# Kernel optimization log

Measured on AMD Instinct MI355X. Metric: run time of the kernel, lower is better.

The kernel has to match this reference:

```python
import jax, jax.numpy as jnp
import numpy as np

B = 4096


def setup_inputs() -> dict:
    key = jax.random.key(0)
    u = jax.random.uniform(key, (B, 5), dtype=jnp.float32)
    centers = u[:, :2] * 64.0          # box centers in [0, 64)
    wh = u[:, 2:4] * 8.0 + 1.0         # widths/heights in [1, 9)
    ang = u[:, 4:5] * 3.14159265       # rotation angle in [0, pi)
    boxes = jnp.concatenate([centers, wh, ang], axis=-1)  # (B,5)
    return {"boxes": boxes}


def _rect_to_corners(boxes):
    # boxes: (B,5) = (x, y, w, h, theta) -> corners (B,4,2)
    unit = jnp.array([[-1.0, -1.0], [1.0, -1.0], [1.0, 1.0], [-1.0, 1.0]],
                     dtype=boxes.dtype)
    ctr, wh, ang = boxes[:, :2], boxes[:, 2:4], boxes[:, 4]
    base = unit[None, :, :] * (wh * 0.5)[:, None, :]        # (B,4,2)
    c, s = jnp.cos(ang), jnp.sin(ang)
    rot = jnp.stack([jnp.stack([c, -s], -1),
                     jnp.stack([s, c], -1)], axis=1)         # (B,2,2)
    return jnp.einsum('bkd,bde->bke', base, rot) + ctr[:, None, :]


def _giou1d(min1, max1, min2, max2):
    # exact (non-fast) 1-D GIoU per axis
    inter = jnp.clip(jnp.minimum(max1, max2) - jnp.maximum(min1, min2), 0.0)
    union = (max1 - min1) + (max2 - min2) - inter
    hull = jnp.maximum(max1, max2) - jnp.minimum(min1, min2)
    return inter / union - (hull - union) / hull


def reference(boxes):
    corners = _rect_to_corners(boxes)                        # (B,4,2)
    nb = corners.shape[0]
    # two edge axes per box: c1-c0 and c3-c0
    axes = jnp.stack([corners[:, 1] - corners[:, 0],
                      corners[:, 3] - corners[:, 0]], axis=1)  # (B,2,2)
    # self projections: box b's corners onto its own axes
    sp = jnp.einsum('bkd,bad->bak', corners, axes)           # (B,2,4)
    smin, smax = sp.min(-1), sp.max(-1)                      # (B,2)
    # cross projections: corners of box i onto axes of box j
    cp = jnp.einsum('ikd,jad->ijak', corners, axes)          # (B,B,2,4)
    cmin, cmax = cp.min(-1), cp.max(-1)                      # (B,B,2)
    # projections of box j's corners onto box i's axes = transpose of cross
    cminT, cmaxT = jnp.swapaxes(cmin, 0, 1), jnp.swapaxes(cmax, 0, 1)
    # axes of box i: (box i self) vs (box j projected on i's axes)
    gA = _giou1d(smin[:, None, :], smax[:, None, :], cminT, cmaxT)  # (B,B,2)
    # axes of box j: (box i projected on j's axes) vs (box j self)
    gB = _giou1d(cmin, cmax, smin[None, :, :], smax[None, :, :])    # (B,B,2)
    g = jnp.concatenate([gA, gB], axis=-1).min(-1)           # min over 4 axes
    pairwise = jnp.clip(g, 0.0)
    idx = jnp.arange(nb)
    pairwise = pairwise.at[idx, idx].set(0.0)                # zero diagonal
    return pairwise  # reduction='none' -> (B,B)
```

## Files before the change

kernel.cpp:

```cpp
#include <hip/hip_runtime.h>
#include <math.h>

#define NBOX 4096
#define TILE 32
#define NT (NBOX / TILE)
#define NBLK (NT * (NT + 1) / 2)
#define SS 12
#define JBASE (TILE * SS)


struct Box {
    float cx, cy, a0x, a0y, a1x, a1y, sc0, sc1, l0, l1;
};

__device__ __forceinline__ float rcp_fast(float x) {
    return __builtin_amdgcn_rcpf(x);
}

__device__ __forceinline__ float giou_axis1(float H1, float H2, float D) {
    float S = H1 + H2;
    float u = fmaf(0.5f, S, -fabsf(D));
    float r = fminf(fminf(H1, H2), u);
    return r * rcp_fast(S - r);
}

__device__ __forceinline__ float mgiou_pair(const Box& I, const Box& J) {
    float d00 = fmaf(I.a0x, J.a0x, I.a0y * J.a0y);
    float d01 = fmaf(I.a0x, J.a1x, I.a0y * J.a1y);
    float d10 = fmaf(I.a1x, J.a0x, I.a1y * J.a0y);
    float d11 = fmaf(I.a1x, J.a1x, I.a1y * J.a1y);
    float DI0 = fmaf(I.a0x, J.cx, fmaf(I.a0y, J.cy, -I.sc0));
    float DI1 = fmaf(I.a1x, J.cx, fmaf(I.a1y, J.cy, -I.sc1));
    float DJ0 = fmaf(J.a0x, I.cx, fmaf(J.a0y, I.cy, -J.sc0));
    float DJ1 = fmaf(J.a1x, I.cx, fmaf(J.a1y, I.cy, -J.sc1));
    float HI0 = fabsf(d00) + fabsf(d01);
    float HI1 = fabsf(d10) + fabsf(d11);
    float HJ0 = fabsf(d00) + fabsf(d10);
    float HJ1 = fabsf(d01) + fabsf(d11);
    float g0 = giou_axis1(I.l0, HI0, DI0);
    float g1 = giou_axis1(I.l1, HI1, DI1);
    float g2 = giou_axis1(J.l0, HJ0, DJ0);
    float g3 = giou_axis1(J.l1, HJ1, DJ1);
    float g = fminf(fminf(g0, g1), fminf(g2, g3));
    return fmaxf(g, 0.0f);
}

__device__ __forceinline__ int j_offset(int j) {
    return JBASE + j * SS + (j >> 3) * 4;
}

__device__ __forceinline__ Box load_box(const float* p) {
    Box b;
    float4 x = *(const float4*)(p);
    float4 y = *(const float4*)(p + 4);
    float2 z = *(const float2*)(p + 8);
    b.cx = x.x;  b.cy = x.y;  b.a0x = x.z; b.a0y = x.w;
    b.a1x = y.x; b.a1y = y.y; b.sc0 = y.z; b.sc1 = y.w;
    b.l0 = z.x;  b.l1 = z.y;
    return b;
}

__global__ __launch_bounds__(256)
void pairwise_kernel(const float* __restrict__ boxes, float* __restrict__ out) {
    int k = blockIdx.x;
    int bi = (int)((float)(2 * NT + 1 - sqrtf((float)((2 * NT + 1) * (2 * NT + 1) - 8 * k))) * 0.5f);
    if (bi > 0 && k < bi * NT - bi * (bi - 1) / 2) bi--;
    if (k >= (bi + 1) * NT - (bi + 1) * bi / 2) bi++;
    int bj = bi + (k - (bi * NT - bi * (bi - 1) / 2));

    __shared__ float sm[JBASE + TILE * SS + 16];
    __shared__ float tileT[TILE][TILE + 1];

    int tid = threadIdx.x;
    if (tid < 2 * TILE) {
        int loc = (tid < TILE) ? tid : (tid - TILE);
        int box = (tid < TILE) ? (bi * TILE + loc) : (bj * TILE + loc);
        float cx = boxes[box * 5 + 0];
        float cy = boxes[box * 5 + 1];
        float w  = boxes[box * 5 + 2];
        float h  = boxes[box * 5 + 3];
        float ang = boxes[box * 5 + 4];
        float s, c;
        __sincosf(ang, &s, &c);
        float a0x = w * c, a0y = -w * s;
        float a1x = h * s, a1y =  h * c;
        float sc0 = fmaf(a0x, cx, a0y * cy);
        float sc1 = fmaf(a1x, cx, a1y * cy);
        float* d = &sm[(tid < TILE) ? (loc * SS) : j_offset(loc)];
        ((float4*)d)[0] = make_float4(cx, cy, a0x, a0y);
        ((float4*)d)[1] = make_float4(a1x, a1y, sc0, sc1);
        ((float2*)d)[4] = make_float2(w * w, h * h);
    }
    __syncthreads();

    int tx = tid & 15;
    int ty = tid >> 4;
    Box I0 = load_box(&sm[ty * SS]);
    Box I1 = load_box(&sm[(ty + 16) * SS]);
    const float* jp = &sm[j_offset(2 * tx)];
    Box J0 = load_box(jp);
    Box J1 = load_box(jp + SS);

    int ibase = bi * TILE, jbase = bj * TILE;
    int ig0 = ibase + ty, ig1 = ig0 + 16;
    int jg0 = jbase + 2 * tx, jg1 = jg0 + 1;

    float v00 = (ig0 == jg0) ? 0.0f : mgiou_pair(I0, J0);
    float v01 = (ig0 == jg1) ? 0.0f : mgiou_pair(I0, J1);
    float v10 = (ig1 == jg0) ? 0.0f : mgiou_pair(I1, J0);
    float v11 = (ig1 == jg1) ? 0.0f : mgiou_pair(I1, J1);

    *(float2*)&out[(size_t)ig0 * NBOX + jg0] = make_float2(v00, v01);
    *(float2*)&out[(size_t)ig1 * NBOX + jg0] = make_float2(v10, v11);

    tileT[ty][2 * tx]          = v00;
    tileT[ty][2 * tx + 1]      = v01;
    tileT[ty + 16][2 * tx]     = v10;
    tileT[ty + 16][2 * tx + 1] = v11;
    __syncthreads();

    #pragma unroll
    for (int dr = 0; dr < 2; ++dr) {
        int jl = ty + dr * 16;
        float2 o = make_float2(tileT[2 * tx][jl], tileT[2 * tx + 1][jl]);
        *(float2*)&out[(size_t)(jbase + jl) * NBOX + ibase + 2 * tx] = o;
    }
}

extern "C" void kernel_launch(void* const* d_in, const int* in_sizes, int n_in,
                              void* d_out, int out_size, void* d_ws, size_t ws_size,
                              hipStream_t stream) {
    const float* boxes = (const float*)d_in[0];
    float* out = (float*)d_out;
    pairwise_kernel<<<dim3(NBLK), dim3(256), 0, stream>>>(boxes, out);
}
```

Measured before the change: 82.11 us.

## Enlarge pair tiles to 64x64 with 4x4 per-thread work and nontemporal stores

Doubles the tile size so each 256-thread block covers a 64x64 pair tile, with each thread computing a 4x4 register block instead of 2x2. This amortises per-block box preprocessing and triangular index math over more pairs, and widens global writes to 16-byte vectors. Output stores use nontemporal hints so the large write-only output bypasses cache. In exchange, register pressure rises and the block count falls to about 2080, which may reduce occupancy and latency hiding.

```diff
diff --git a/kernel.cpp b/kernel.cpp
--- a/kernel.cpp
+++ b/kernel.cpp
@@ -2,11 +2,13 @@
 #include <math.h>
 
 #define NBOX 4096
-#define TILE 32
+#define TILE 64
 #define NT (NBOX / TILE)
 #define NBLK (NT * (NT + 1) / 2)
 #define SS 12
 #define JBASE (TILE * SS)
+
+typedef float vfloat4 __attribute__((ext_vector_type(4)));
 
 
 struct Box {
@@ -68,13 +70,13 @@
     if (k >= (bi + 1) * NT - (bi + 1) * bi / 2) bi++;
     int bj = bi + (k - (bi * NT - bi * (bi - 1) / 2));
 
-    __shared__ float sm[JBASE + TILE * SS + 16];
+    __shared__ float sm[JBASE + TILE * SS + ((TILE - 1) >> 3) * 4 + 8];
     __shared__ float tileT[TILE][TILE + 1];
 
     int tid = threadIdx.x;
     if (tid < 2 * TILE) {
-        int loc = (tid < TILE) ? tid : (tid - TILE);
-        int box = (tid < TILE) ? (bi * TILE + loc) : (bj * TILE + loc);
+        int loc = tid & (TILE - 1);
+        int box = ((tid < TILE) ? bi : bj) * TILE + loc;
         float cx = boxes[box * 5 + 0];
         float cy = boxes[box * 5 + 1];
         float w  = boxes[box * 5 + 2];
@@ -95,35 +97,45 @@
 
     int tx = tid & 15;
     int ty = tid >> 4;
-    Box I0 = load_box(&sm[ty * SS]);
-    Box I1 = load_box(&sm[(ty + 16) * SS]);
-    const float* jp = &sm[j_offset(2 * tx)];
-    Box J0 = load_box(jp);
-    Box J1 = load_box(jp + SS);
+    Box I[4], J[4];
+    #pragma unroll
+    for (int kk = 0; kk < 4; ++kk) I[kk] = load_box(&sm[(ty + 16 * kk) * SS]);
+    const float* jp = &sm[j_offset(4 * tx)];
+    #pragma unroll
+    for (int m = 0; m < 4; ++m) J[m] = load_box(jp + m * SS);
 
     int ibase = bi * TILE, jbase = bj * TILE;
-    int ig0 = ibase + ty, ig1 = ig0 + 16;
-    int jg0 = jbase + 2 * tx, jg1 = jg0 + 1;
+    float v[4][4];
+    #pragma unroll
+    for (int kk = 0; kk < 4; ++kk) {
+        int ig = ibase + ty + 16 * kk;
+        #pragma unroll
+        for (int m = 0; m < 4; ++m) {
+            int jg = jbase + 4 * tx + m;
+            v[kk][m] = (ig == jg) ? 0.0f : mgiou_pair(I[kk], J[m]);
+        }
+    }
 
-    float v00 = (ig0 == jg0) ? 0.0f : mgiou_pair(I0, J0);
-    float v01 = (ig0 == jg1) ? 0.0f : mgiou_pair(I0, J1);
-    float v10 = (ig1 == jg0) ? 0.0f : mgiou_pair(I1, J0);
-    float v11 = (ig1 == jg1) ? 0.0f : mgiou_pair(I1, J1);
+    #pragma unroll
+    for (int kk = 0; kk < 4; ++kk) {
+        int ig = ibase + ty + 16 * kk;
+        vfloat4 o = {v[kk][0], v[kk][1], v[kk][2], v[kk][3]};
+        __builtin_nontemporal_store(o, (vfloat4*)&out[(size_t)ig * NBOX + jbase + 4 * tx]);
+    }
 
-    *(float2*)&out[(size_t)ig0 * NBOX + jg0] = make_float2(v00, v01);
-    *(float2*)&out[(size_t)ig1 * NBOX + jg0] = make_float2(v10, v11);
-
-    tileT[ty][2 * tx]          = v00;
-    tileT[ty][2 * tx + 1]      = v01;
-    tileT[ty + 16][2 * tx]     = v10;
-    tileT[ty + 16][2 * tx + 1] = v11;
+    #pragma unroll
+    for (int kk = 0; kk < 4; ++kk)
+        #pragma unroll
+        for (int m = 0; m < 4; ++m)
+            tileT[ty + 16 * kk][4 * tx + m] = v[kk][m];
     __syncthreads();
 
     #pragma unroll
-    for (int dr = 0; dr < 2; ++dr) {
-        int jl = ty + dr * 16;
-        float2 o = make_float2(tileT[2 * tx][jl], tileT[2 * tx + 1][jl]);
-        *(float2*)&out[(size_t)(jbase + jl) * NBOX + ibase + 2 * tx] = o;
+    for (int kk = 0; kk < 4; ++kk) {
+        int jl = ty + 16 * kk;
+        vfloat4 o = {tileT[4 * tx + 0][jl], tileT[4 * tx + 1][jl],
+                     tileT[4 * tx + 2][jl], tileT[4 * tx + 3][jl]};
+        __builtin_nontemporal_store(o, (vfloat4*)&out[(size_t)(jbase + jl) * NBOX + ibase + 4 * tx]);
     }
 }
 
```

Result: no change. 81.99 us (-0.1%).
